# Kernel tuning notes

Hardware: AMD Instinct MI355X
Metric: run time of the kernel (lower is better)

Reference implementation:

```python
import jax, jax.numpy as jnp
import numpy as np

N, K, C_IN, H, W = 32, 17, 2048, 64, 64
POSEMB, HID, NLAYERS = 64, 128, 4
IMG = jnp.array([1920.0, 1080.0, 1920.0, 1080.0], jnp.float32)  # image_width/height from img_metas
# H36M 17-joint skeleton edges
EDGES = [(0,1),(1,2),(2,3),(0,4),(4,5),(5,6),(0,7),(7,8),(8,9),(9,10),(8,11),(11,12),(12,13),(8,14),(14,15),(15,16)]
_m = np.eye(K, dtype=bool)
for _i, _j in EDGES:
    _m[_i, _j] = _m[_j, _i] = True
ADJ_MASK = jnp.asarray(_m)
EYE = jnp.eye(K, dtype=jnp.float32)
BN_EPS = 1e-5


def semgconv(x, Wp, b, E):
    # SemGraphConv: separate weights for self (W[0]) and neighbor (W[1]) paths,
    # learned edge logits E masked to the skeleton and row-softmaxed.
    h0 = jnp.einsum('bkc,cd->bkd', x, Wp[0])
    h1 = jnp.einsum('bkc,cd->bkd', x, Wp[1])
    adj = jax.nn.softmax(jnp.where(ADJ_MASK, E, -9e15), axis=1)
    return (jnp.einsum('ij,bjd->bid', adj * EYE, h0)
            + jnp.einsum('ij,bjd->bid', adj * (1.0 - EYE), h1) + b)


def bn_relu(x, gamma, beta):
    # BatchNorm1d in eval mode with running_mean=0, running_var=1, then ReLU.
    return jax.nn.relu(x * gamma * jax.lax.rsqrt(jnp.float32(1.0 + BN_EPS)) + beta)


def setup_inputs() -> dict:
    key = jax.random.key(0)
    ks = jax.random.split(key, 12)
    C_emb = POSEMB + C_IN  # 2112
    NG = 2 * NLAYERS       # 8 hidden graph convs (4 residual blocks x 2)
    return {
        'x': jax.random.normal(ks[0], (N, C_IN, H, W), jnp.float32),
        'heatmap': jax.random.uniform(ks[1], (N, K, H, W), jnp.float32),
        'bbox': jax.random.uniform(ks[2], (N, 4), jnp.float32) * IMG,
        'pos_w': jax.random.normal(ks[3], (6, POSEMB), jnp.float32) * 0.2,
        'pos_b': jnp.zeros((POSEMB,), jnp.float32),
        'Wi': jax.random.normal(ks[4], (2, C_emb, HID), jnp.float32) * 0.02,
        'bi': jnp.zeros((HID,), jnp.float32),
        'Ei': jax.random.normal(ks[5], (K, K), jnp.float32),
        'gi': jnp.ones((HID,), jnp.float32),
        'bti': jnp.zeros((HID,), jnp.float32),
        'Wh': jax.random.normal(ks[6], (NG, 2, HID, HID), jnp.float32) * 0.05,
        'bh': jnp.zeros((NG, HID), jnp.float32),
        'Eh': jax.random.normal(ks[7], (NG, K, K), jnp.float32),
        'gh': jnp.ones((NG, HID), jnp.float32),
        'bth': jnp.zeros((NG, HID), jnp.float32),
        'Wo': jax.random.normal(ks[8], (2, HID, 3), jnp.float32) * 0.05,
        'bo': jnp.zeros((3,), jnp.float32),
        'Eo': jax.random.normal(ks[9], (K, K), jnp.float32),
    }


def reference(x, heatmap, bbox, pos_w, pos_b, Wi, bi, Ei, gi, bti, Wh, bh, Eh, gh, bth, Wo, bo, Eo):
    # get_keypoint: argmax over flattened heatmap -> (kx, ky), normalized to [-1,1]
    loc = jnp.argmax(heatmap.reshape(N, K, H * W), axis=2)          # [N,K] flat index ky*W+kx
    kx = (loc % W).astype(jnp.float32)
    ky = (loc // W).astype(jnp.float32)
    kp = jnp.stack([kx / W * 2.0 - 1.0, ky / H * 2.0 - 1.0], axis=-1)  # [N,K,2]
    # get_bbox: normalize by image size, first two coords -> [-1,1], broadcast over K
    bnrm = bbox / IMG
    bnrm = jnp.concatenate([bnrm[:, :2] * 2.0 - 1.0, bnrm[:, 2:]], axis=1)
    bb = jnp.broadcast_to(bnrm[:, None, :], (N, K, 4))
    # posemb MLP (single Linear(6, 64) since posemb_dim=[64])
    posemb = jnp.concatenate([kp, bb], axis=2) @ pos_w + pos_b      # [N,K,64]
    # featemb: vectorized replacement of the per-(i,j) Python-loop gather x[i,:,ky,kx]
    featemb = jnp.take_along_axis(x.reshape(N, C_IN, H * W), loc[:, None, :], axis=2)
    featemb = featemb.transpose(0, 2, 1)                            # [N,K,2048]
    h = jnp.concatenate([posemb, featemb], axis=2)                  # [N,K,2112]
    # SemGCN: input gconv + BN + ReLU, 4 residual blocks, output gconv
    h = bn_relu(semgconv(h, Wi, bi, Ei), gi, bti)
    for l in range(NLAYERS):
        r = h
        for s in range(2):
            i = 2 * l + s
            r = bn_relu(semgconv(r, Wh[i], bh[i], Eh[i]), gh[i], bth[i])
        h = h + r
    return semgconv(h, Wo, bo, Eo)                                  # [N,K,3]
```

## Files before the change

### kernel.cpp

```cpp
#include <hip/hip_runtime.h>

#define NB    32
#define KJ    17
#define CIN   2048
#define HWSZ  4096
#define WDIM  64
#define CEMB  2112
#define HID   128
#define NROWS (NB*KJ)
#define SPLITK 4

__device__ __constant__ unsigned c_mask[KJ] = {
  0x00093u, 0x00007u, 0x0000Eu, 0x0000Cu, 0x00031u, 0x00070u, 0x00060u,
  0x00181u, 0x04B80u, 0x00700u, 0x00600u, 0x01900u, 0x03800u, 0x03000u,
  0x0C100u, 0x1C000u, 0x18000u
};

__device__ __forceinline__ float fma4(const float4 s, const float4 wv, float a) {
  return fmaf(s.x, wv.x, fmaf(s.y, wv.y, fmaf(s.z, wv.z, fmaf(s.w, wv.w, a))));
}

__global__ __launch_bounds__(256) void k_front(
    const float* __restrict__ heatmap, const float* __restrict__ bbox,
    const float* __restrict__ pos_w, const float* __restrict__ pos_b,
    const float* __restrict__ Wi, const float* __restrict__ Wh,
    const float* __restrict__ x, float* __restrict__ h_ws,
    float4* __restrict__ Wpi4, float4* __restrict__ Wph4) {
  const int blk = blockIdx.x;
  const int t = threadIdx.x;

  if (blk >= NROWS) {
    const int pb = blk - NROWS;
    if (pb < 528) {
      const int idx4 = pb * 256 + t;
      const int d = idx4 & 127, rest = idx4 >> 7;
      const int c4 = rest % 528, p = rest / 528;
      const float* src = Wi + ((size_t)(p * CEMB + c4 * 4)) * HID + d;
      Wpi4[((size_t)p * 528 + c4) * 128 + d] =
          make_float4(src[0], src[HID], src[2 * HID], src[3 * HID]);
    } else {
      const int idx4 = (pb - 528) * 256 + t;
      const int d = idx4 & 127, rest = idx4 >> 7;
      const int c4 = rest & 31, lp = rest >> 5;
      const float* src = Wh + ((size_t)(lp * HID + c4 * 4)) * HID + d;
      Wph4[((size_t)lp * 32 + c4) * 128 + d] =
          make_float4(src[0], src[HID], src[2 * HID], src[3 * HID]);
    }
    return;
  }

  const int b = blk;
  const int n = b / KJ;
  __shared__ float svals[256];
  __shared__ int   sidx[256];

  const float4* hm4 = (const float4*)(heatmap + (size_t)b * HWSZ);
  float best = -1e30f; int bidx = 0;
  #pragma unroll
  for (int k = 0; k < 4; ++k) {
    const int vi = k * 256 + t;
    const float4 v = hm4[vi];
    const int base = vi * 4;
    if (v.x > best) { best = v.x; bidx = base;     }
    if (v.y > best) { best = v.y; bidx = base + 1; }
    if (v.z > best) { best = v.z; bidx = base + 2; }
    if (v.w > best) { best = v.w; bidx = base + 3; }
  }
  svals[t] = best; sidx[t] = bidx;
  __syncthreads();
  for (int s = 128; s > 0; s >>= 1) {
    if (t < s) {
      const float v2 = svals[t + s]; const int i2 = sidx[t + s];
      if (v2 > svals[t] || (v2 == svals[t] && i2 < sidx[t])) {
        svals[t] = v2; sidx[t] = i2;
      }
    }
    __syncthreads();
  }
  const int loc = sidx[0];

  if (t < 64) {
    const float kx = (float)(loc & (WDIM - 1));
    const float ky = (float)(loc >> 6);
    float in6[6];
    in6[0] = kx * (2.0f / 64.0f) - 1.0f;
    in6[1] = ky * (2.0f / 64.0f) - 1.0f;
    in6[2] = bbox[n * 4 + 0] * (2.0f / 1920.0f) - 1.0f;
    in6[3] = bbox[n * 4 + 1] * (2.0f / 1080.0f) - 1.0f;
    in6[4] = bbox[n * 4 + 2] * (1.0f / 1920.0f);
    in6[5] = bbox[n * 4 + 3] * (1.0f / 1080.0f);
    float acc = pos_b[t];
    #pragma unroll
    for (int c = 0; c < 6; ++c) acc = fmaf(in6[c], pos_w[c * 64 + t], acc);
    h_ws[(size_t)b * CEMB + t] = acc;
  }

  const float* xn = x + (size_t)n * CIN * HWSZ + loc;
  float* hrow = h_ws + (size_t)b * CEMB + 64;
  #pragma unroll
  for (int k = 0; k < 8; ++k) {
    const int c = k * 256 + t;
    hrow[c] = xn[(size_t)c * HWSZ];
  }
}

__global__ __launch_bounds__(256) void k_gemm_in(
    const float* __restrict__ Wpi_f, const float* __restrict__ h_ws,
    float* __restrict__ part) {
  const int bm = blockIdx.x, bn = blockIdx.y, bz = blockIdx.z;
  const int t = threadIdx.x;
  const int lane = t & 63, g = t >> 6;
  const int j = bn * 64 + lane;
  const int p = j >> 7, d = j & 127;
  const int row0 = bm * 16;

  const float4* W4 = (const float4*)Wpi_f + ((size_t)p * 528 + bz * 132) * 128 + d;
  const int k0 = bz * 528;

  __shared__ float At[16][48];
  float acc[4] = {0.f, 0.f, 0.f, 0.f};
  float4 ws[3];

  ws[0] = W4[0];
  ws[1] = W4[128];

  for (int st = 0; st < 11; ++st) {
    const int kk = k0 + st * 48;
    __syncthreads();
    for (int idx = t; idx < 16 * 48; idx += 256) {
      const int r = idx / 48, c = idx - r * 48;
      At[r][c] = h_ws[(size_t)(row0 + r) * CEMB + kk + c];
    }
    __syncthreads();
    #pragma unroll
    for (int u = 0; u < 12; ++u) {
      {
        int pf = st * 12 + u + 2;
        pf = pf < 132 ? pf : 131;
        ws[(u + 2) % 3] = W4[(size_t)pf * 128];
      }
      const float4 wv = ws[u % 3];
      #pragma unroll
      for (int r = 0; r < 4; ++r) {
        const float4 s = *(const float4*)&At[g * 4 + r][u * 4];
        acc[r] = fma4(s, wv, acc[r]);
      }
    }
  }
  #pragma unroll
  for (int r = 0; r < 4; ++r) {
    part[((size_t)bz * NROWS + row0 + g * 4 + r) * 256 + j] = acc[r];
  }
}

__device__ __forceinline__ void layer4s(
    const float (*S)[HID], const float4* __restrict__ W0,
    const float4* __restrict__ W1, float (*O0)[HID], float (*O1)[HID],
    int q, int j) {
  const int r0 = q * 5;
  float a0[5] = {0.f, 0.f, 0.f, 0.f, 0.f};
  float a1[5] = {0.f, 0.f, 0.f, 0.f, 0.f};
  float4 w0s[4], w1s[4];

  #pragma unroll
  for (int u = 0; u < 3; ++u) {
    w0s[u] = W0[u * 128 + j];
    w1s[u] = W1[u * 128 + j];
  }
  #pragma unroll
  for (int cc = 0; cc < 32; ++cc) {
    if (cc < 29) {
      w0s[(cc + 3) % 4] = W0[(cc + 3) * 128 + j];
      w1s[(cc + 3) % 4] = W1[(cc + 3) * 128 + j];
    }
    const float4 wv0 = w0s[cc % 4];
    const float4 wv1 = w1s[cc % 4];
    #pragma unroll
    for (int r = 0; r < 5; ++r) {
      const float4 s = *(const float4*)&S[r0 + r][cc * 4];
      a0[r] = fma4(s, wv0, a0[r]);
      a1[r] = fma4(s, wv1, a1[r]);
    }
  }
  #pragma unroll
  for (int r = 0; r < 5; ++r) { O0[r0 + r][j] = a0[r]; O1[r0 + r][j] = a1[r]; }
}

template <int ADD>
__device__ __forceinline__ void mix_bn2(
    const float (*T0)[HID], const float (*T1)[HID], const float (*A)[KJ],
    float pb, float pg, float pt, float (*dst)[HID], int q, int d) {
  const float gsv = pg * 0.99999500003749969f;
  for (int i = q; i < KJ; i += 4) {
    float s = 0.f;
    #pragma unroll
    for (int jj = 0; jj < KJ; ++jj) s = fmaf(A[i][jj], T1[jj][d], s);
    s += A[i][i] * (T0[i][d] - T1[i][d]);
    const float v = fmaxf(fmaf(s + pb, gsv, pt), 0.f);
    if (ADD) dst[i][d] += v; else dst[i][d] = v;
  }
}

__global__ __launch_bounds__(512) void k_gcn(
    const float* __restrict__ part,
    const float* __restrict__ Ei, const float* __restrict__ bi,
    const float* __restrict__ gi, const float* __restrict__ bti,
    const float* __restrict__ Wph, const float* __restrict__ bh,
    const float* __restrict__ Eh, const float* __restrict__ gh,
    const float* __restrict__ bth, const float* __restrict__ Wo,
    const float* __restrict__ bo, const float* __restrict__ Eo,
    float* __restrict__ out) {
  __shared__ float adjm[10][KJ][KJ];
  __shared__ float Hs[20][HID], Rs[20][HID], T0s[20][HID], T1s[20][HID];
  const int n = blockIdx.x, t = threadIdx.x;
  const int q = t >> 7, j = t & 127;

  const float ibb = bi[j], igg = gi[j], ibt = bti[j];

  if (t < 170) {
    const int m = t / KJ, i = t % KJ;
    const float* Es = (m == 0) ? Ei : ((m <= 8) ? Eh + (size_t)(m - 1) * KJ * KJ : Eo);
    const unsigned msk = c_mask[i];
    float mx = -1e30f;
    #pragma unroll
    for (int jj = 0; jj < KJ; ++jj)
      if (msk & (1u << jj)) mx = fmaxf(mx, Es[i * KJ + jj]);
    float ev[KJ];
    float sum = 0.f;
    #pragma unroll
    for (int jj = 0; jj < KJ; ++jj) {
      const float e = (msk & (1u << jj)) ? expf(Es[i * KJ + jj] - mx) : 0.f;
      ev[jj] = e; sum += e;
    }
    const float inv = 1.f / sum;
    #pragma unroll
    for (int jj = 0; jj < KJ; ++jj) adjm[m][i][jj] = ev[jj] * inv;
  }
  if (t < 384) { Hs[17 + (t >> 7)][t & 127] = 0.f; Rs[17 + (t >> 7)][t & 127] = 0.f; }

  {
    const float* p0 = part + (size_t)(n * KJ) * 256;
    for (int idx = t; idx < KJ * 256; idx += 512) {
      const int k = idx >> 8, jj = idx & 255;
      float v = 0.f;
      #pragma unroll
      for (int z = 0; z < SPLITK; ++z)
        v += p0[(size_t)z * NROWS * 256 + k * 256 + jj];
      if (jj < HID) T0s[k][jj] = v; else T1s[k][jj - HID] = v;
    }
  }
  __syncthreads();

  mix_bn2<0>(T0s, T1s, adjm[0], ibb, igg, ibt, Hs, q, j);
  __syncthreads();

  const float4* Wp4 = (const float4*)Wph;
  for (int l = 0; l < 4; ++l) {
    const int iA = 2 * l, iB = 2 * l + 1;
    {
      const float pb = bh[iA * HID + j], pg = gh[iA * HID + j], pt = bth[iA * HID + j];
      layer4s(Hs, Wp4 + (size_t)(iA * 2) * 4096, Wp4 + (size_t)(iA * 2 + 1) * 4096,
              T0s, T1s, q, j);
      __syncthreads();
      mix_bn2<0>(T0s, T1s, adjm[1 + iA], pb, pg, pt, Rs, q, j);
      __syncthreads();
    }
    {
      const float pb = bh[iB * HID + j], pg = gh[iB * HID + j], pt = bth[iB * HID + j];
      layer4s(Rs, Wp4 + (size_t)(iB * 2) * 4096, Wp4 + (size_t)(iB * 2 + 1) * 4096,
              T0s, T1s, q, j);
      __syncthreads();
      mix_bn2<1>(T0s, T1s, adjm[1 + iB], pb, pg, pt, Hs, q, j);
      __syncthreads();
    }
  }

  if (t < 102) {
    const int p = t / 51, rem = t % 51, i = rem / 3, e = rem % 3;
    const float* Wp = Wo + p * HID * 3 + e;
    float s = 0.f;
    #pragma unroll 4
    for (int c = 0; c < HID; ++c) s = fmaf(Hs[i][c], Wp[c * 3], s);
    if (p == 0) T0s[i][e] = s; else T1s[i][e] = s;
  }
  __syncthreads();
  if (t < 51) {
    const int i = t / 3, e = t % 3;
    const float (*A)[KJ] = adjm[9];
    float s = bo[e];
    #pragma unroll
    for (int jj = 0; jj < KJ; ++jj) s = fmaf(A[i][jj], T1s[jj][e], s);
    s += A[i][i] * (T0s[i][e] - T1s[i][e]);
    out[(n * KJ + i) * 3 + e] = s;
  }
}

extern "C" void kernel_launch(void* const* d_in, const int* in_sizes, int n_in,
                              void* d_out, int out_size, void* d_ws, size_t ws_size,
                              hipStream_t stream) {
  const float* x       = (const float*)d_in[0];
  const float* heatmap = (const float*)d_in[1];
  const float* bbox    = (const float*)d_in[2];
  const float* pos_w   = (const float*)d_in[3];
  const float* pos_b   = (const float*)d_in[4];
  const float* Wi      = (const float*)d_in[5];
  const float* bi      = (const float*)d_in[6];
  const float* Ei      = (const float*)d_in[7];
  const float* gi      = (const float*)d_in[8];
  const float* bti     = (const float*)d_in[9];
  const float* Wh      = (const float*)d_in[10];
  const float* bh      = (const float*)d_in[11];
  const float* Eh      = (const float*)d_in[12];
  const float* gh      = (const float*)d_in[13];
  const float* bth     = (const float*)d_in[14];
  const float* Wo      = (const float*)d_in[15];
  const float* bo      = (const float*)d_in[16];
  const float* Eo      = (const float*)d_in[17];
  float* out = (float*)d_out;

  float* h_ws = (float*)d_ws;
  float* part = h_ws + (size_t)NROWS * CEMB;
  float* Wpi  = part + (size_t)SPLITK * NROWS * 256;
  float* Wph  = Wpi + (size_t)2 * CEMB * HID;

  k_front<<<NROWS + 528 + 256, 256, 0, stream>>>(
      heatmap, bbox, pos_w, pos_b, Wi, Wh, x, h_ws,
      (float4*)Wpi, (float4*)Wph);
  k_gemm_in<<<dim3(34, 4, SPLITK), 256, 0, stream>>>(Wpi, h_ws, part);
  k_gcn<<<NB, 512, 0, stream>>>(part, Ei, bi, gi, bti, Wph, bh, Eh, gh, bth,
                                Wo, bo, Eo, out);
}
```

Measured before the change: 132.3 us.

## Fuse input graph-conv GEMM into per-sample GCN kernel with 1024 threads

Removes the separate split-K input GEMM kernel and its partial-sum buffer. Each of the 32 GCN blocks now computes its own 17x2112 by 2112x256 input projection, staging h rows through shared memory. The block grows to 1024 threads so the self and neighbor weight paths run on separate thread halves, in that GEMM and in the hidden layers. This saves one launch and the partial-sum round trip through global memory. The cost is that the largest GEMM now runs on only 32 blocks instead of 544, so each block streams the full 2.1 MB input weight matrix and most CUs sit idle.

```diff
diff --git a/kernel.cpp b/kernel.cpp
--- a/kernel.cpp
+++ b/kernel.cpp
@@ -8,7 +8,6 @@
 #define CEMB  2112
 #define HID   128
 #define NROWS (NB*KJ)
-#define SPLITK 4
 
 __device__ __constant__ unsigned c_mask[KJ] = {
   0x00093u, 0x00007u, 0x0000Eu, 0x0000Cu, 0x00031u, 0x00070u, 0x00060u,
@@ -104,94 +103,30 @@
   }
 }
 
-__global__ __launch_bounds__(256) void k_gemm_in(
-    const float* __restrict__ Wpi_f, const float* __restrict__ h_ws,
-    float* __restrict__ part) {
-  const int bm = blockIdx.x, bn = blockIdx.y, bz = blockIdx.z;
-  const int t = threadIdx.x;
-  const int lane = t & 63, g = t >> 6;
-  const int j = bn * 64 + lane;
-  const int p = j >> 7, d = j & 127;
-  const int row0 = bm * 16;
-
-  const float4* W4 = (const float4*)Wpi_f + ((size_t)p * 528 + bz * 132) * 128 + d;
-  const int k0 = bz * 528;
-
-  __shared__ float At[16][48];
-  float acc[4] = {0.f, 0.f, 0.f, 0.f};
-  float4 ws[3];
-
-  ws[0] = W4[0];
-  ws[1] = W4[128];
-
-  for (int st = 0; st < 11; ++st) {
-    const int kk = k0 + st * 48;
-    __syncthreads();
-    for (int idx = t; idx < 16 * 48; idx += 256) {
-      const int r = idx / 48, c = idx - r * 48;
-      At[r][c] = h_ws[(size_t)(row0 + r) * CEMB + kk + c];
-    }
-    __syncthreads();
-    #pragma unroll
-    for (int u = 0; u < 12; ++u) {
-      {
-        int pf = st * 12 + u + 2;
-        pf = pf < 132 ? pf : 131;
-        ws[(u + 2) % 3] = W4[(size_t)pf * 128];
-      }
-      const float4 wv = ws[u % 3];
-      #pragma unroll
-      for (int r = 0; r < 4; ++r) {
-        const float4 s = *(const float4*)&At[g * 4 + r][u * 4];
-        acc[r] = fma4(s, wv, acc[r]);
-      }
-    }
-  }
-  #pragma unroll
-  for (int r = 0; r < 4; ++r) {
-    part[((size_t)bz * NROWS + row0 + g * 4 + r) * 256 + j] = acc[r];
-  }
-}
-
-__device__ __forceinline__ void layer4s(
-    const float (*S)[HID], const float4* __restrict__ W0,
-    const float4* __restrict__ W1, float (*O0)[HID], float (*O1)[HID],
-    int q, int j) {
-  const int r0 = q * 5;
-  float a0[5] = {0.f, 0.f, 0.f, 0.f, 0.f};
-  float a1[5] = {0.f, 0.f, 0.f, 0.f, 0.f};
-  float4 w0s[4], w1s[4];
-
-  #pragma unroll
-  for (int u = 0; u < 3; ++u) {
-    w0s[u] = W0[u * 128 + j];
-    w1s[u] = W1[u * 128 + j];
-  }
+__device__ __forceinline__ void layer_p(
+    const float (*S)[HID], const float4* __restrict__ Wp,
+    float (*Op)[HID], int r0, int j) {
+  float a[5] = {0.f, 0.f, 0.f, 0.f, 0.f};
+  float4 ws[4];
+  ws[0] = Wp[j]; ws[1] = Wp[128 + j]; ws[2] = Wp[256 + j];
   #pragma unroll
   for (int cc = 0; cc < 32; ++cc) {
-    if (cc < 29) {
-      w0s[(cc + 3) % 4] = W0[(cc + 3) * 128 + j];
-      w1s[(cc + 3) % 4] = W1[(cc + 3) * 128 + j];
-    }
-    const float4 wv0 = w0s[cc % 4];
-    const float4 wv1 = w1s[cc % 4];
-    #pragma unroll
-    for (int r = 0; r < 5; ++r) {
-      const float4 s = *(const float4*)&S[r0 + r][cc * 4];
-      a0[r] = fma4(s, wv0, a0[r]);
-      a1[r] = fma4(s, wv1, a1[r]);
-    }
-  }
-  #pragma unroll
-  for (int r = 0; r < 5; ++r) { O0[r0 + r][j] = a0[r]; O1[r0 + r][j] = a1[r]; }
+    if (cc < 29) ws[(cc + 3) % 4] = Wp[(cc + 3) * 128 + j];
+    const float4 wv = ws[cc % 4];
+    #pragma unroll
+    for (int r = 0; r < 5; ++r)
+      a[r] = fma4(*(const float4*)&S[r0 + r][cc * 4], wv, a[r]);
+  }
+  #pragma unroll
+  for (int r = 0; r < 5; ++r) Op[r0 + r][j] = a[r];
 }
 
 template <int ADD>
 __device__ __forceinline__ void mix_bn2(
     const float (*T0)[HID], const float (*T1)[HID], const float (*A)[KJ],
-    float pb, float pg, float pt, float (*dst)[HID], int q, int d) {
+    float pb, float pg, float pt, float (*dst)[HID], int g, int d) {
   const float gsv = pg * 0.99999500003749969f;
-  for (int i = q; i < KJ; i += 4) {
+  for (int i = g; i < KJ; i += 8) {
     float s = 0.f;
     #pragma unroll
     for (int jj = 0; jj < KJ; ++jj) s = fmaf(A[i][jj], T1[jj][d], s);
@@ -201,8 +136,8 @@
   }
 }
 
-__global__ __launch_bounds__(512) void k_gcn(
-    const float* __restrict__ part,
+__global__ __launch_bounds__(1024) void k_gcn(
+    const float* __restrict__ h_ws, const float* __restrict__ Wpi,
     const float* __restrict__ Ei, const float* __restrict__ bi,
     const float* __restrict__ gi, const float* __restrict__ bti,
     const float* __restrict__ Wph, const float* __restrict__ bh,
@@ -212,10 +147,20 @@
     float* __restrict__ out) {
   __shared__ float adjm[10][KJ][KJ];
   __shared__ float Hs[20][HID], Rs[20][HID], T0s[20][HID], T1s[20][HID];
+  __shared__ float At[20][96];
   const int n = blockIdx.x, t = threadIdx.x;
-  const int q = t >> 7, j = t & 127;
+  const int p = t >> 9;
+  const int qq = (t >> 7) & 3;
+  const int j = t & 127;
+  const int g = t >> 7;
+  const int r0 = qq * 5;
 
   const float ibb = bi[j], igg = gi[j], ibt = bti[j];
+  float pbh[8], pgh[8], pth[8];
+  #pragma unroll
+  for (int i = 0; i < 8; ++i) {
+    pbh[i] = bh[i * HID + j]; pgh[i] = gh[i * HID + j]; pth[i] = bth[i * HID + j];
+  }
 
   if (t < 170) {
     const int m = t / KJ, i = t % KJ;
@@ -237,51 +182,65 @@
     for (int jj = 0; jj < KJ; ++jj) adjm[m][i][jj] = ev[jj] * inv;
   }
   if (t < 384) { Hs[17 + (t >> 7)][t & 127] = 0.f; Rs[17 + (t >> 7)][t & 127] = 0.f; }
+  if (t >= 384 && t < 672) {
+    const int u = t - 384;
+    At[17 + u / 96][u % 96] = 0.f;
+  }
 
   {
-    const float* p0 = part + (size_t)(n * KJ) * 256;
-    for (int idx = t; idx < KJ * 256; idx += 512) {
-      const int k = idx >> 8, jj = idx & 255;
-      float v = 0.f;
+    const float* hn = h_ws + (size_t)(n * KJ) * CEMB;
+    const float4* W4 = (const float4*)Wpi + (size_t)p * (528 * 128) + j;
+    float acc[5] = {0.f, 0.f, 0.f, 0.f, 0.f};
+    float4 wr[3];
+    wr[0] = W4[0];
+    wr[1] = W4[128];
+    for (int st = 0; st < 22; ++st) {
+      __syncthreads();
+      for (int idx = t; idx < KJ * 96; idx += 1024) {
+        const int r = idx / 96, c = idx - r * 96;
+        At[r][c] = hn[(size_t)r * CEMB + st * 96 + c];
+      }
+      __syncthreads();
       #pragma unroll
-      for (int z = 0; z < SPLITK; ++z)
-        v += p0[(size_t)z * NROWS * 256 + k * 256 + jj];
-      if (jj < HID) T0s[k][jj] = v; else T1s[k][jj - HID] = v;
-    }
-  }
-  __syncthreads();
-
-  mix_bn2<0>(T0s, T1s, adjm[0], ibb, igg, ibt, Hs, q, j);
+      for (int u = 0; u < 24; ++u) {
+        const int ci = st * 24 + u;
+        const int pf = (ci + 2 < 528) ? ci + 2 : 527;
+        wr[(u + 2) % 3] = W4[(size_t)pf * 128];
+        const float4 wv = wr[u % 3];
+        #pragma unroll
+        for (int r = 0; r < 5; ++r)
+          acc[r] = fma4(*(const float4*)&At[r0 + r][u * 4], wv, acc[r]);
+      }
+    }
+    float (*Tp)[HID] = p ? T1s : T0s;
+    #pragma unroll
+    for (int r = 0; r < 5; ++r) Tp[r0 + r][j] = acc[r];
+  }
+  __syncthreads();
+
+  mix_bn2<0>(T0s, T1s, adjm[0], ibb, igg, ibt, Hs, g, j);
   __syncthreads();
 
   const float4* Wp4 = (const float4*)Wph;
   for (int l = 0; l < 4; ++l) {
     const int iA = 2 * l, iB = 2 * l + 1;
-    {
-      const float pb = bh[iA * HID + j], pg = gh[iA * HID + j], pt = bth[iA * HID + j];
-      layer4s(Hs, Wp4 + (size_t)(iA * 2) * 4096, Wp4 + (size_t)(iA * 2 + 1) * 4096,
-              T0s, T1s, q, j);
-      __syncthreads();
-      mix_bn2<0>(T0s, T1s, adjm[1 + iA], pb, pg, pt, Rs, q, j);
-      __syncthreads();
-    }
-    {
-      const float pb = bh[iB * HID + j], pg = gh[iB * HID + j], pt = bth[iB * HID + j];
-      layer4s(Rs, Wp4 + (size_t)(iB * 2) * 4096, Wp4 + (size_t)(iB * 2 + 1) * 4096,
-              T0s, T1s, q, j);
-      __syncthreads();
-      mix_bn2<1>(T0s, T1s, adjm[1 + iB], pb, pg, pt, Hs, q, j);
-      __syncthreads();
-    }
+    layer_p(Hs, Wp4 + (size_t)(iA * 2 + p) * 4096, p ? T1s : T0s, r0, j);
+    __syncthreads();
+    mix_bn2<0>(T0s, T1s, adjm[1 + iA], pbh[iA], pgh[iA], pth[iA], Rs, g, j);
+    __syncthreads();
+    layer_p(Rs, Wp4 + (size_t)(iB * 2 + p) * 4096, p ? T1s : T0s, r0, j);
+    __syncthreads();
+    mix_bn2<1>(T0s, T1s, adjm[1 + iB], pbh[iB], pgh[iB], pth[iB], Hs, g, j);
+    __syncthreads();
   }
 
   if (t < 102) {
-    const int p = t / 51, rem = t % 51, i = rem / 3, e = rem % 3;
-    const float* Wp = Wo + p * HID * 3 + e;
+    const int pp = t / 51, rem = t % 51, i = rem / 3, e = rem % 3;
+    const float* Wp = Wo + pp * HID * 3 + e;
     float s = 0.f;
     #pragma unroll 4
     for (int c = 0; c < HID; ++c) s = fmaf(Hs[i][c], Wp[c * 3], s);
-    if (p == 0) T0s[i][e] = s; else T1s[i][e] = s;
+    if (pp == 0) T0s[i][e] = s; else T1s[i][e] = s;
   }
   __syncthreads();
   if (t < 51) {
@@ -319,14 +278,12 @@
   float* out = (float*)d_out;
 
   float* h_ws = (float*)d_ws;
-  float* part = h_ws + (size_t)NROWS * CEMB;
-  float* Wpi  = part + (size_t)SPLITK * NROWS * 256;
+  float* Wpi  = h_ws + (size_t)NROWS * CEMB;
   float* Wph  = Wpi + (size_t)2 * CEMB * HID;
 
   k_front<<<NROWS + 528 + 256, 256, 0, stream>>>(
       heatmap, bbox, pos_w, pos_b, Wi, Wh, x, h_ws,
       (float4*)Wpi, (float4*)Wph);
-  k_gemm_in<<<dim3(34, 4, SPLITK), 256, 0, stream>>>(Wpi, h_ws, part);
-  k_gcn<<<NB, 512, 0, stream>>>(part, Ei, bi, gi, bti, Wph, bh, Eh, gh, bth,
-                                Wo, bo, Eo, out);
-}
+  k_gcn<<<NB, 1024, 0, stream>>>(h_ws, Wpi, Ei, bi, gi, bti, Wph, bh, Eh, gh,
+                                 bth, Wo, bo, Eo, out);
+}
```

Result: slower. 237.4 us (+79.4%).
